# Performance work log

Measured on AMD Instinct MI355X. Metric: run time of the kernel, lower is better.

## Reference

```python
import jax, jax.numpy as jnp
import numpy as np

# module hyperparams (match init_kwargs)
C_IN = 256
HEADS = 8
HEAD_DIM = 32
PW, PH = 4, 4
TOPK = 2
SIM_POW = 2.0
SIDE = 64
T = SIDE * SIDE
B = 16


def setup_inputs() -> dict:
    key = jax.random.key(0)
    ks = jax.random.split(key, 7)
    hd = HEADS * HEAD_DIM
    s = 1.0 / np.sqrt(C_IN)
    return {
        "x": jax.random.normal(ks[0], (T, B, C_IN), dtype=jnp.float32),
        "f_w": jax.random.uniform(ks[1], (hd, C_IN), jnp.float32, -s, s),
        "f_b": jax.random.uniform(ks[2], (hd,), jnp.float32, -s, s),
        "v_w": jax.random.uniform(ks[3], (hd, C_IN), jnp.float32, -s, s),
        "v_b": jax.random.uniform(ks[4], (hd,), jnp.float32, -s, s),
        "proj_w": jax.random.uniform(ks[5], (C_IN, hd), jnp.float32, -1.0 / np.sqrt(hd), 1.0 / np.sqrt(hd)),
        "proj_b": jax.random.uniform(ks[6], (C_IN,), jnp.float32, -1.0 / np.sqrt(hd), 1.0 / np.sqrt(hd)),
        "sim_alpha": jnp.ones((1,), jnp.float32),
        "sim_beta": jnp.zeros((1,), jnp.float32),
    }


def _l2norm(z):
    # F.normalize with eps=1e-12
    n = jnp.linalg.norm(z, axis=-1, keepdims=True)
    return z / jnp.maximum(n, 1e-12)


def reference(x, f_w, f_b, v_w, v_b, proj_w, proj_b, sim_alpha, sim_beta):
    t, b, c = x.shape
    side = SIDE
    H, D = HEADS, HEAD_DIM
    M = PW * PH

    xt = jnp.transpose(x, (1, 0, 2))  # [B, T, C]
    q = xt @ f_w.T + f_b              # [B, T, H*D] (1x1 conv)
    v = xt @ v_w.T + v_b

    def split_heads(z):
        # [B,T,H*D] -> [B*H, side, side, D]
        z = z.reshape(b, side, side, H, D)
        return jnp.transpose(z, (0, 3, 1, 2, 4)).reshape(b * H, side, side, D)

    q2 = split_heads(q)
    v2 = split_heads(v)

    def pool(z):
        # adaptive avg pool (side,side)->(PW,PH), side divisible by PW/PH
        z = z.reshape(b * H, PW, side // PW, PH, side // PH, D)
        return z.mean(axis=(2, 4)).reshape(b * H, M, D)

    centers = pool(q2)        # [BH, M, D]
    value_centers = pool(v2)  # [BH, M, D]
    q_tok = q2.reshape(b * H, t, D)
    v_tok = v2.reshape(b * H, t, D)

    sim = jax.nn.sigmoid(
        sim_beta + sim_alpha * jnp.einsum("bmd,btd->bmt", _l2norm(centers), _l2norm(q_tok))
    )  # [BH, M, T]

    k = min(TOPK, M)
    _, idx = jax.lax.top_k(jnp.transpose(sim, (0, 2, 1)), k)  # idx [BH, T, k] over centers
    mask = jax.nn.one_hot(idx, M, dtype=sim.dtype).sum(axis=2)  # [BH, T, M]
    sim = sim * jnp.transpose(mask, (0, 2, 1))
    if SIM_POW != 1.0:
        sim = sim ** SIM_POW
    sim = sim / (sim.sum(axis=1, keepdims=True) + 1e-6)

    centers_out = (jnp.einsum("bmt,btd->bmd", sim, v_tok) + value_centers) / (
        sim.sum(axis=2, keepdims=True) + 1.0
    )  # [BH, M, D]
    out_tok = jnp.einsum("bmt,bmd->btd", sim, centers_out)  # [BH, T, D]

    out = jnp.transpose(out_tok.reshape(b, H, side, side, D), (0, 2, 3, 1, 4)).reshape(b, t, H * D)
    out = out @ proj_w.T + proj_b  # [B, T, C]
    return jnp.transpose(out, (1, 0, 2))  # [T, B, C]
```

## Files before the change

### kernel.cpp

```cpp
#include <hip/hip_runtime.h>
#include <math.h>

#define T_SZ 4096
#define B_SZ 16
#define CIN 256
#define N_H 8
#define D_H 32
#define M_C 16
#define TAU 5e-5f
#define RCAP (1<<19)

typedef unsigned char u8;
typedef unsigned int uint;
typedef unsigned short ushort;

using frag_ab = __attribute__((ext_vector_type(8))) short;
using frag_c  = __attribute__((ext_vector_type(4))) float;

#define O_FWT   0
#define O_VWT   262144
#define O_WFH   524288
#define O_WFL   655360
#define O_WVH   786432
#define O_WVL   917504
#define O_WPH   1048576
#define O_WPL   1179648
#define O_PX    1310720
#define O_C64   1835008
#define O_C32   2359296
#define O_VC    2621440
#define O_COUT  2883584
#define O_GPART 3145728
#define O_CNT   5308416
#define O_LIST  5308672
#define O_SELM  7405824
#define O_SELW  8454400
#define O_V     12648704

__device__ __forceinline__ uint bfr(float f){
  uint u = __float_as_uint(f);
  return (u + 0x7FFFu + ((u >> 16) & 1u)) >> 16;
}
__device__ __forceinline__ float bff(uint h){ return __uint_as_float(h << 16); }

__global__ void k_transpose(const float* __restrict__ fw, const float* __restrict__ vw,
                            float* __restrict__ fwT, float* __restrict__ vwT){
  int id = blockIdx.x * 256 + threadIdx.x;
  int mat = id >> 16; int rem = id & 65535;
  int j = rem >> 8, c = rem & 255;
  const float* src = (mat == 0) ? fw : vw;
  float* dst = (mat == 0) ? fwT : vwT;
  dst[c * 256 + j] = src[j * 256 + c];
}

__global__ void k_wsplit(const float* __restrict__ fw, const float* __restrict__ vw,
                         const float* __restrict__ pw,
                         ushort* __restrict__ fh, ushort* __restrict__ fl,
                         ushort* __restrict__ vh, ushort* __restrict__ vl,
                         ushort* __restrict__ ph, ushort* __restrict__ pl){
  int id = blockIdx.x * 256 + threadIdx.x;
  int mat = id >> 16, rem = id & 65535;
  const float* s = (mat == 0) ? fw : ((mat == 1) ? vw : pw);
  ushort* dh = (mat == 0) ? fh : ((mat == 1) ? vh : ph);
  ushort* dl = (mat == 0) ? fl : ((mat == 1) ? vl : pl);
  float a = s[rem];
  uint h = bfr(a);
  dh[rem] = (ushort)h;
  dl[rem] = (ushort)bfr(a - bff(h));
}

__global__ void k_pool(const float* __restrict__ x, double* __restrict__ px){
  int b = blockIdx.x >> 4, m = blockIdx.x & 15;
  int pr = m >> 2, pc = m & 3;
  int c = threadIdx.x;
  double s = 0.0;
  for (int i = 0; i < 16; i++){
    int t0 = (pr * 16 + i) * 64 + pc * 16;
    const float* xr = x + ((size_t)t0 * B_SZ + b) * CIN + c;
    for (int jj = 0; jj < 16; jj++)
      s += (double)xr[(size_t)jj * B_SZ * CIN];
  }
  px[(size_t)(b * 16 + m) * 256 + c] = s * (1.0 / 256.0);
}

__global__ void k_centers(const double* __restrict__ px, const float* __restrict__ fwT,
                          const float* __restrict__ vwT, const float* __restrict__ fb,
                          const float* __restrict__ vb, double* __restrict__ c64,
                          float* __restrict__ c32, float* __restrict__ vc){
  int b = blockIdx.x >> 4, m = blockIdx.x & 15;
  int j = threadIdx.x;
  const double* pxr = px + (size_t)(b * 16 + m) * 256;
  double cq = (double)fb[j], cv = (double)vb[j];
  for (int c = 0; c < 256; c++){
    double p = pxr[c];
    cq += p * (double)fwT[c * 256 + j];
    cv += p * (double)vwT[c * 256 + j];
  }
  __shared__ double sq[256];
  __shared__ double snm[8];
  sq[j] = cq * cq;
  __syncthreads();
  int h = j >> 5, d = j & 31;
  if ((j & 31) == 0){
    double ts = 0.0;
    for (int dd = 0; dd < 32; dd++) ts += sq[h * 32 + dd];
    snm[h] = fmax(sqrt(ts), 1e-12);
  }
  __syncthreads();
  double nm = snm[h];
  size_t o = ((size_t)(b * N_H + h) * M_C + m) * D_H + d;
  double ch = cq / nm;
  c64[o] = ch; c32[o] = (float)ch; vc[o] = (float)cv;
}

#define LSTR 40
#define LTILE (128 * LSTR)

__device__ __forceinline__ void stage_tiles(
    const float* __restrict__ A, size_t aBase, int aStride, int kk,
    const ushort* __restrict__ Bh, const ushort* __restrict__ Bl,
    ushort* Ah, ushort* Al, ushort* Bhs, ushort* Bls, int tid){
#pragma unroll
  for (int rep = 0; rep < 2; rep++){
    int part = tid + rep * 256;
    int row = part >> 2, q4 = part & 3;
    const float* ga = A + aBase + (size_t)row * aStride + kk * 32 + q4 * 8;
    float4 a0 = *(const float4*)ga;
    float4 a1 = *(const float4*)(ga + 4);
    uint h0 = bfr(a0.x), h1 = bfr(a0.y), h2 = bfr(a0.z), h3 = bfr(a0.w);
    uint h4 = bfr(a1.x), h5 = bfr(a1.y), h6 = bfr(a1.z), h7 = bfr(a1.w);
    uint l0 = bfr(a0.x - bff(h0)), l1 = bfr(a0.y - bff(h1));
    uint l2 = bfr(a0.z - bff(h2)), l3 = bfr(a0.w - bff(h3));
    uint l4 = bfr(a1.x - bff(h4)), l5 = bfr(a1.y - bff(h5));
    uint l6 = bfr(a1.z - bff(h6)), l7 = bfr(a1.w - bff(h7));
    uint4 hv = make_uint4(h0 | (h1 << 16), h2 | (h3 << 16), h4 | (h5 << 16), h6 | (h7 << 16));
    uint4 lv = make_uint4(l0 | (l1 << 16), l2 | (l3 << 16), l4 | (l5 << 16), l6 | (l7 << 16));
    *(uint4*)&Ah[row * LSTR + q4 * 8] = hv;
    *(uint4*)&Al[row * LSTR + q4 * 8] = lv;
    size_t bo = (size_t)row * 256 + kk * 32 + q4 * 8;
    *(uint4*)&Bhs[row * LSTR + q4 * 8] = *(const uint4*)(Bh + bo);
    *(uint4*)&Bls[row * LSTR + q4 * 8] = *(const uint4*)(Bl + bo);
  }
}

__device__ __forceinline__ void compute_step(
    const ushort* Ah, const ushort* Al, const ushort* Bhs, const ushort* Bls,
    int wm, int wn, int li, int quad, frag_c acc[4][4]){
  frag_ab ah[4], al[4], bh[4], bl[4];
#pragma unroll
  for (int m = 0; m < 4; m++){
    int off = (wm * 64 + m * 16 + li) * LSTR + quad * 8;
    ah[m] = *(const frag_ab*)&Ah[off];
    al[m] = *(const frag_ab*)&Al[off];
  }
#pragma unroll
  for (int n = 0; n < 4; n++){
    int off = (wn * 64 + n * 16 + li) * LSTR + quad * 8;
    bh[n] = *(const frag_ab*)&Bhs[off];
    bl[n] = *(const frag_ab*)&Bls[off];
  }
#pragma unroll
  for (int m = 0; m < 4; m++)
#pragma unroll
    for (int n = 0; n < 4; n++){
      acc[m][n] = __builtin_amdgcn_mfma_f32_16x16x32_bf16(ah[m], bh[n], acc[m][n], 0, 0, 0);
      acc[m][n] = __builtin_amdgcn_mfma_f32_16x16x32_bf16(ah[m], bl[n], acc[m][n], 0, 0, 0);
      acc[m][n] = __builtin_amdgcn_mfma_f32_16x16x32_bf16(al[m], bh[n], acc[m][n], 0, 0, 0);
    }
}

__device__ __forceinline__ void gemm_core(
    const float* __restrict__ A, size_t aBase, int aStride,
    const ushort* __restrict__ Bh, const ushort* __restrict__ Bl,
    ushort* SM, frag_c acc[4][4], int tid){
  ushort* Ah = SM;             ushort* Al = SM + LTILE;
  ushort* Bhs = SM + 2*LTILE;  ushort* Bls = SM + 3*LTILE;
  int li = tid & 15, quad = (tid & 63) >> 4;
  int w = tid >> 6, wm = w >> 1, wn = w & 1;
#pragma unroll
  for (int m = 0; m < 4; m++)
#pragma unroll
    for (int n = 0; n < 4; n++)
      acc[m][n] = frag_c{0.f, 0.f, 0.f, 0.f};
  for (int kk = 0; kk < 8; kk++){
    __syncthreads();
    stage_tiles(A, aBase, aStride, kk, Bh, Bl, Ah, Al, Bhs, Bls, tid);
    __syncthreads();
    compute_step(Ah, Al, Bhs, Bls, wm, wn, li, quad, acc);
  }
}

__global__ __launch_bounds__(256, 3) void k_gemm_store(
    const float* __restrict__ A, int aStride, int aBMul,
    const ushort* __restrict__ Bh, const ushort* __restrict__ Bl,
    const float* __restrict__ bias,
    float* __restrict__ Out, int oStride, int oBMul){
  int bx = blockIdx.x;
  int nt = bx & 1, mt = (bx >> 1) & 31, b = bx >> 6;
  __shared__ ushort SM[4 * LTILE];
  frag_c acc[4][4];
  int tid = threadIdx.x;
  size_t aBase = (size_t)b * aBMul + (size_t)(mt * 128) * aStride;
  const ushort* Bhp = Bh + (size_t)(nt * 128) * 256;
  const ushort* Blp = Bl + (size_t)(nt * 128) * 256;
  gemm_core(A, aBase, aStride, Bhp, Blp, SM, acc, tid);

  int li = tid & 15, quad = (tid & 63) >> 4;
  int w = tid >> 6, wm = w >> 1, wn = w & 1;
  int colBase = nt * 128 + wn * 64 + li;
  float bn[4];
#pragma unroll
  for (int n = 0; n < 4; n++) bn[n] = bias[colBase + n * 16];
#pragma unroll
  for (int m = 0; m < 4; m++){
    int row0 = mt * 128 + wm * 64 + m * 16 + quad * 4;
#pragma unroll
    for (int n = 0; n < 4; n++){
      int col = colBase + n * 16;
#pragma unroll
      for (int r = 0; r < 4; r++)
        Out[(size_t)(row0 + r) * oStride + (size_t)b * oBMul + col] = acc[m][n][r] + bn[n];
    }
  }
}

__global__ __launch_bounds__(256, 2) void k_gemm_qsim(
    const float* __restrict__ A, int aStride, int aBMul,
    const ushort* __restrict__ Bh, const ushort* __restrict__ Bl,
    const float* __restrict__ bias, const float* __restrict__ c32,
    const float* __restrict__ salpha, const float* __restrict__ sbeta,
    u8* __restrict__ selm, float2* __restrict__ selw,
    int* __restrict__ cnt, unsigned int* __restrict__ list){
  int bx = blockIdx.x;
  int nt = bx & 1, mt = (bx >> 1) & 31, b = bx >> 6;
  __shared__ ushort SM[4 * LTILE];
  __shared__ float cs[4][520];
  frag_c acc[4][4];
  int tid = threadIdx.x;
  for (int i = tid; i < 2048; i += 256){
    int hh = i >> 9, rem = i & 511;
    cs[hh][rem] = c32[(size_t)b * 4096 + (nt * 4 + hh) * 512 + rem];
  }
  size_t aBase = (size_t)b * aBMul + (size_t)(mt * 128) * aStride;
  const ushort* Bhp = Bh + (size_t)(nt * 128) * 256;
  const ushort* Blp = Bl + (size_t)(nt * 128) * 256;
  gemm_core(A, aBase, aStride, Bhp, Blp, SM, acc, tid);

  int li = tid & 15, quad = (tid & 63) >> 4;
  int w = tid >> 6, wm = w >> 1, wn = w & 1;
  int colBase = nt * 128 + wn * 64 + li;
  float bn[4];
#pragma unroll
  for (int n = 0; n < 4; n++) bn[n] = bias[colBase + n * 16];
  float alpha = salpha[0], beta = sbeta[0];
  float* qbuf = (float*)SM;
  for (int half = 0; half < 2; half++){
    __syncthreads();
    if (wm == half){
#pragma unroll
      for (int m = 0; m < 4; m++)
#pragma unroll
        for (int n = 0; n < 4; n++)
#pragma unroll
          for (int r = 0; r < 4; r++)
            qbuf[(m * 16 + quad * 4 + r) * 132 + wn * 64 + n * 16 + li] = acc[m][n][r] + bn[n];
    }
    __syncthreads();
    int tok = tid >> 2, hh = tid & 3;
    int t = mt * 128 + half * 64 + tok;
    int h = nt * 4 + hh;
    float q[32];
    float ss = 0.f;
#pragma unroll
    for (int d = 0; d < 32; d += 4){
      float4 qv = *(const float4*)&qbuf[tok * 132 + hh * 32 + d];
      q[d] = qv.x; q[d + 1] = qv.y; q[d + 2] = qv.z; q[d + 3] = qv.w;
      ss += qv.x * qv.x + qv.y * qv.y + qv.z * qv.z + qv.w * qv.w;
    }
    float inv = 1.f / fmaxf(sqrtf(ss), 1e-12f);
    float s1 = -1e30f, s2 = -1e30f, s3 = -1e30f; int i1 = 0, i2 = 0;
#pragma unroll
    for (int m = 0; m < 16; m++){
      float dot = 0.f;
#pragma unroll
      for (int d = 0; d < 32; d += 4){
        float4 cv = *(const float4*)&cs[hh][m * 32 + d];
        dot = fmaf(q[d], cv.x, fmaf(q[d + 1], cv.y, fmaf(q[d + 2], cv.z, fmaf(q[d + 3], cv.w, dot))));
      }
      float z = beta + alpha * (dot * inv);
      float s = 1.f / (1.f + expf(-z));
      if (s > s1){ s3 = s2; s2 = s1; i2 = i1; s1 = s; i1 = m; }
      else if (s > s2){ s3 = s2; s2 = s; i2 = m; }
      else if (s > s3){ s3 = s; }
    }
    if (s2 - s3 < TAU){
      int idx = atomicAdd(cnt, 1);
      if (idx < RCAP) list[idx] = (((unsigned)(b * N_H + h)) << 12) | (unsigned)t;
    }
    float r1 = s1 * s1, r2 = s2 * s2;
    float den = r1 + r2 + 1e-6f;
    size_t so = (size_t)(b * N_H + h) * T_SZ + t;
    selm[so * 2] = (u8)i1; selm[so * 2 + 1] = (u8)i2;
    selw[so] = make_float2(r1 / den, r2 / den);
  }
}

__global__ __launch_bounds__(256, 4) void k_rescue(
    const float* __restrict__ x, const float* __restrict__ fw, const float* __restrict__ fb,
    const double* __restrict__ c64, const float* __restrict__ salpha, const float* __restrict__ sbeta,
    const int* __restrict__ cnt, const unsigned int* __restrict__ list,
    u8* __restrict__ selm, float2* __restrict__ selw){
  int n = *cnt; if (n > RCAP) n = RCAP;
  int lane = threadIdx.x & 63;
  int wid = (blockIdx.x * 256 + threadIdx.x) >> 6;
  int nw = gridDim.x * 4;
  double alpha = (double)salpha[0], beta = (double)sbeta[0];
  for (int i = wid; i < n; i += nw){
    unsigned e = list[i];
    int t = e & 4095; int bh = e >> 12; int b = bh >> 3, h = bh & 7;
    int d = lane & 31, half = lane >> 5;
    const float* xh = x + ((size_t)t * B_SZ + b) * CIN + half * 128;
    const float* wr = fw + (size_t)(h * 32 + d) * CIN + half * 128;
    double a0 = 0, a1 = 0, a2 = 0, a3 = 0;
#pragma unroll 4
    for (int c = 0; c < 128; c += 4){
      float4 xv = *(const float4*)(xh + c);
      float4 wv = *(const float4*)(wr + c);
      a0 += (double)xv.x * (double)wv.x;
      a1 += (double)xv.y * (double)wv.y;
      a2 += (double)xv.z * (double)wv.z;
      a3 += (double)xv.w * (double)wv.w;
    }
    double qd = (a0 + a1) + (a2 + a3);
    qd += __shfl_down(qd, 32);
    if (lane < 32) qd += (double)fb[h * 32 + d];
    else qd = 0.0;
    double ss = qd * qd;
#pragma unroll
    for (int off = 32; off; off >>= 1) ss += __shfl_xor(ss, off);
    double inv = 1.0 / fmax(sqrt(ss), 1e-12);
    const double* cb = c64 + (size_t)bh * (M_C * D_H);
    int m = lane & 15;
    double dot = 0.0;
#pragma unroll
    for (int dd = 0; dd < 32; dd++){
      double qv = __shfl(qd, dd);
      dot += qv * cb[m * 32 + dd];
    }
    double z = beta + alpha * (dot * inv);
    double s = 1.0 / (1.0 + exp(-z));
    double s1 = -1e300, s2 = -1e300; int i1 = 0, i2 = 0;
#pragma unroll
    for (int mm = 0; mm < 16; mm++){
      double sv = __shfl(s, mm);
      if (sv > s1){ s2 = s1; i2 = i1; s1 = sv; i1 = mm; }
      else if (sv > s2){ s2 = sv; i2 = mm; }
    }
    if (lane == 0){
      double r1 = s1 * s1, r2 = s2 * s2, den = r1 + r2 + 1e-6;
      size_t so = (size_t)bh * T_SZ + t;
      selm[so * 2] = (u8)i1; selm[so * 2 + 1] = (u8)i2;
      selw[so] = make_float2((float)(r1 / den), (float)(r2 / den));
    }
  }
}

__global__ __launch_bounds__(256, 4) void k_scatter(
    const float* __restrict__ v, const u8* __restrict__ selm, const float2* __restrict__ selw,
    float* __restrict__ gpart){
  int bh = blockIdx.x >> 3, chunk = blockIdx.x & 7;
  int b = bh >> 3, h = bh & 7;
  int tid = threadIdx.x;
  int mA = tid >> 5, mB = mA + 8, d = tid & 31;
  __shared__ uchar2 sm[512];
  __shared__ float2 sw[512];
  for (int i = tid; i < 512; i += 256){
    size_t so = (size_t)bh * T_SZ + chunk * 512 + i;
    sm[i] = make_uchar2(selm[so * 2], selm[so * 2 + 1]);
    sw[i] = selw[so];
  }
  __syncthreads();
  const float* vb = v + ((size_t)b * T_SZ + chunk * 512) * CIN + h * 32 + d;
  float accA = 0.f, accB = 0.f, cntA = 0.f, cntB = 0.f;
#pragma unroll 8
  for (int i = 0; i < 512; i++){
    float vv = vb[(size_t)i * CIN];
    uchar2 mm = sm[i];
    float2 w = sw[i];
    float wA = (mm.x == mA) ? w.x : ((mm.y == mA) ? w.y : 0.f);
    float wB = (mm.x == mB) ? w.x : ((mm.y == mB) ? w.y : 0.f);
    accA = fmaf(wA, vv, accA); cntA += wA;
    accB = fmaf(wB, vv, accB); cntB += wB;
  }
  float* gp = gpart + (size_t)(bh * 8 + chunk) * 528;
  gp[mA * 33 + d] = accA;
  gp[mB * 33 + d] = accB;
  if (d == 0){ gp[mA * 33 + 32] = cntA; gp[mB * 33 + 32] = cntB; }
}

__global__ void k_cfinal(const float* __restrict__ gpart, const float* __restrict__ vc,
                         float* __restrict__ cout){
  int id = blockIdx.x * 256 + threadIdx.x;
  int bh = id >> 9, rem = id & 511, m = rem >> 5, d = rem & 31;
  float num = 0.f, den = 0.f;
#pragma unroll
  for (int c = 0; c < 8; c++){
    const float* gp = gpart + (size_t)(bh * 8 + c) * 528 + m * 33;
    num += gp[d];
    den += gp[32];
  }
  cout[id] = (num + vc[id]) / (den + 1.0f);
}

__global__ __launch_bounds__(256, 4) void k_mix(
    const float* __restrict__ cout, const u8* __restrict__ selm, const float2* __restrict__ selw,
    float* __restrict__ OT){
  int b = blockIdx.x >> 7, tt = blockIdx.x & 127;
  __shared__ float cs[8][516];
  int tid = threadIdx.x;
  for (int k = 0; k < 16; k++){
    int i = k * 256 + tid;
    cs[i >> 9][i & 511] = cout[(size_t)b * 4096 + i];
  }
  __syncthreads();
  int r = tid >> 3, h = tid & 7;
  int t = tt * 32 + r;
  size_t so = (size_t)(b * N_H + h) * T_SZ + t;
  int m1 = selm[so * 2], m2 = selm[so * 2 + 1];
  float2 w = selw[so];
#pragma unroll
  for (int d = 0; d < 32; d += 4){
    float4 c1 = *(const float4*)&cs[h][m1 * 32 + d];
    float4 c2 = *(const float4*)&cs[h][m2 * 32 + d];
    float4 o = make_float4(w.x * c1.x + w.y * c2.x, w.x * c1.y + w.y * c2.y,
                           w.x * c1.z + w.y * c2.z, w.x * c1.w + w.y * c2.w);
    *(float4*)&OT[((size_t)b * T_SZ + t) * CIN + h * 32 + d] = o;
  }
}

extern "C" void kernel_launch(void* const* d_in, const int* in_sizes, int n_in,
                              void* d_out, int out_size, void* d_ws, size_t ws_size,
                              hipStream_t stream) {
  const float* x   = (const float*)d_in[0];
  const float* f_w = (const float*)d_in[1];
  const float* f_b = (const float*)d_in[2];
  const float* v_w = (const float*)d_in[3];
  const float* v_b = (const float*)d_in[4];
  const float* p_w = (const float*)d_in[5];
  const float* p_b = (const float*)d_in[6];
  const float* s_a = (const float*)d_in[7];
  const float* s_b = (const float*)d_in[8];
  float* out = (float*)d_out;
  char* ws = (char*)d_ws;

  float*  fwT  = (float*)(ws + O_FWT);
  float*  vwT  = (float*)(ws + O_VWT);
  ushort* wfh  = (ushort*)(ws + O_WFH);
  ushort* wfl  = (ushort*)(ws + O_WFL);
  ushort* wvh  = (ushort*)(ws + O_WVH);
  ushort* wvl  = (ushort*)(ws + O_WVL);
  ushort* wph  = (ushort*)(ws + O_WPH);
  ushort* wpl  = (ushort*)(ws + O_WPL);
  double* px   = (double*)(ws + O_PX);
  double* c64  = (double*)(ws + O_C64);
  float*  c32  = (float*)(ws + O_C32);
  float*  vc   = (float*)(ws + O_VC);
  float*  cout = (float*)(ws + O_COUT);
  float*  gpart= (float*)(ws + O_GPART);
  int*    cnt  = (int*)(ws + O_CNT);
  unsigned int* list = (unsigned int*)(ws + O_LIST);
  u8*     selm = (u8*)(ws + O_SELM);
  float2* selw = (float2*)(ws + O_SELW);
  float*  v    = (float*)(ws + O_V);
  float*  OT   = (float*)(ws + O_V);

  hipMemsetAsync(ws + O_CNT, 0, 256, stream);
  k_transpose<<<512, 256, 0, stream>>>(f_w, v_w, fwT, vwT);
  k_wsplit<<<768, 256, 0, stream>>>(f_w, v_w, p_w, wfh, wfl, wvh, wvl, wph, wpl);
  k_pool<<<256, 256, 0, stream>>>(x, px);
  k_centers<<<256, 256, 0, stream>>>(px, fwT, vwT, f_b, v_b, c64, c32, vc);
  k_gemm_qsim<<<1024, 256, 0, stream>>>(x, 4096, 256, wfh, wfl, f_b, c32, s_a, s_b,
                                        selm, selw, cnt, list);
  k_gemm_store<<<1024, 256, 0, stream>>>(x, 4096, 256, wvh, wvl, v_b, v, 256, T_SZ * CIN);
  k_rescue<<<256, 256, 0, stream>>>(x, f_w, f_b, c64, s_a, s_b, cnt, list, selm, selw);
  k_scatter<<<1024, 256, 0, stream>>>(v, selm, selw, gpart);
  k_cfinal<<<256, 256, 0, stream>>>(gpart, vc, cout);
  k_mix<<<2048, 256, 0, stream>>>(cout, selm, selw, OT);
  k_gemm_store<<<1024, 256, 0, stream>>>(OT, 256, T_SZ * CIN, wph, wpl, p_b, out, 4096, 256);
}
```

Measured before the change: 399.4 us.

## Pre-split activations to bf16 hi/lo and stage GEMM tiles via direct global-to-LDS loads

A new pass converts x into bf16 high/low planes in batch-major layout once, and k_mix writes its output directly as bf16 hi/lo, so the GEMM kernels no longer convert fp32 tiles during staging. Tile staging now uses global_load_lds so each wave copies one of the four operand tiles straight into LDS in a k-chunk-major layout, without a register round trip. The cost is an extra full pass over x that writes two 32 MB buffers, plus a larger workspace. Synchronisation is still a plain load-then-barrier with no double buffering.

```diff
diff --git a/kernel.cpp b/kernel.cpp
--- a/kernel.cpp
+++ b/kernel.cpp
@@ -35,7 +35,9 @@
 #define O_LIST  5308672
 #define O_SELM  7405824
 #define O_SELW  8454400
-#define O_V     12648704
+#define O_XS    12648704
+#define O_XSL   46203136
+#define O_V     79757568
 
 __device__ __forceinline__ uint bfr(float f){
   uint u = __float_as_uint(f);
@@ -69,6 +71,20 @@
   dl[rem] = (ushort)bfr(a - bff(h));
 }
 
+__global__ __launch_bounds__(256, 8) void k_xsplit(
+    const float* __restrict__ x, ushort* __restrict__ xh, ushort* __restrict__ xl){
+  size_t gid = (size_t)blockIdx.x * 256 + threadIdx.x;
+  size_t o = gid * 4;
+  int c = (int)(o & 255); size_t bt = o >> 8;
+  int t = (int)(bt & 4095); int b = (int)(bt >> 12);
+  float4 a = *(const float4*)(x + ((size_t)t * B_SZ + b) * CIN + c);
+  uint h0 = bfr(a.x), h1 = bfr(a.y), h2 = bfr(a.z), h3 = bfr(a.w);
+  uint l0 = bfr(a.x - bff(h0)), l1 = bfr(a.y - bff(h1));
+  uint l2 = bfr(a.z - bff(h2)), l3 = bfr(a.w - bff(h3));
+  *(uint2*)(xh + o) = make_uint2(h0 | (h1 << 16), h2 | (h3 << 16));
+  *(uint2*)(xl + o) = make_uint2(l0 | (l1 << 16), l2 | (l3 << 16));
+}
+
 __global__ void k_pool(const float* __restrict__ x, double* __restrict__ px){
   int b = blockIdx.x >> 4, m = blockIdx.x & 15;
   int pr = m >> 2, pc = m & 3;
@@ -113,51 +129,42 @@
   c64[o] = ch; c32[o] = (float)ch; vc[o] = (float)cv;
 }
 
-#define LSTR 40
-#define LTILE (128 * LSTR)
-
-__device__ __forceinline__ void stage_tiles(
-    const float* __restrict__ A, size_t aBase, int aStride, int kk,
-    const ushort* __restrict__ Bh, const ushort* __restrict__ Bl,
-    ushort* Ah, ushort* Al, ushort* Bhs, ushort* Bls, int tid){
-#pragma unroll
-  for (int rep = 0; rep < 2; rep++){
-    int part = tid + rep * 256;
-    int row = part >> 2, q4 = part & 3;
-    const float* ga = A + aBase + (size_t)row * aStride + kk * 32 + q4 * 8;
-    float4 a0 = *(const float4*)ga;
-    float4 a1 = *(const float4*)(ga + 4);
-    uint h0 = bfr(a0.x), h1 = bfr(a0.y), h2 = bfr(a0.z), h3 = bfr(a0.w);
-    uint h4 = bfr(a1.x), h5 = bfr(a1.y), h6 = bfr(a1.z), h7 = bfr(a1.w);
-    uint l0 = bfr(a0.x - bff(h0)), l1 = bfr(a0.y - bff(h1));
-    uint l2 = bfr(a0.z - bff(h2)), l3 = bfr(a0.w - bff(h3));
-    uint l4 = bfr(a1.x - bff(h4)), l5 = bfr(a1.y - bff(h5));
-    uint l6 = bfr(a1.z - bff(h6)), l7 = bfr(a1.w - bff(h7));
-    uint4 hv = make_uint4(h0 | (h1 << 16), h2 | (h3 << 16), h4 | (h5 << 16), h6 | (h7 << 16));
-    uint4 lv = make_uint4(l0 | (l1 << 16), l2 | (l3 << 16), l4 | (l5 << 16), l6 | (l7 << 16));
-    *(uint4*)&Ah[row * LSTR + q4 * 8] = hv;
-    *(uint4*)&Al[row * LSTR + q4 * 8] = lv;
-    size_t bo = (size_t)row * 256 + kk * 32 + q4 * 8;
-    *(uint4*)&Bhs[row * LSTR + q4 * 8] = *(const uint4*)(Bh + bo);
-    *(uint4*)&Bls[row * LSTR + q4 * 8] = *(const uint4*)(Bl + bo);
+#define TSZU 4096
+
+__device__ __forceinline__ void stage_async(
+    const ushort* __restrict__ Ahg, const ushort* __restrict__ Alg, size_t aRow0,
+    const ushort* __restrict__ Bhg, const ushort* __restrict__ Blg, int bRow0,
+    int kk, ushort* SM, int tid){
+  int w = tid >> 6, lane = tid & 63;
+  const ushort* src = (w == 0) ? Ahg : (w == 1) ? Alg : (w == 2) ? Bhg : Blg;
+  size_t row0 = (w < 2) ? aRow0 : (size_t)bRow0;
+  ushort* dst = SM + w * TSZU;
+#pragma unroll
+  for (int j = 0; j < 8; j++){
+    int kchunk = j >> 1, rh = j & 1;
+    const ushort* g = src + (row0 + (size_t)(rh * 64 + lane)) * 256 + kk * 32 + kchunk * 8;
+    ushort* l = dst + (kchunk * 128 + rh * 64) * 8;
+    __builtin_amdgcn_global_load_lds((const __attribute__((address_space(1))) void*)g,
+                                     (__attribute__((address_space(3))) void*)l, 16, 0, 0);
   }
 }
 
 __device__ __forceinline__ void compute_step(
-    const ushort* Ah, const ushort* Al, const ushort* Bhs, const ushort* Bls,
-    int wm, int wn, int li, int quad, frag_c acc[4][4]){
+    const ushort* SM, int wm, int wn, int li, int quad, frag_c acc[4][4]){
+  const ushort* Ah = SM;            const ushort* Al = SM + TSZU;
+  const ushort* Bh = SM + 2*TSZU;   const ushort* Bl = SM + 3*TSZU;
   frag_ab ah[4], al[4], bh[4], bl[4];
 #pragma unroll
   for (int m = 0; m < 4; m++){
-    int off = (wm * 64 + m * 16 + li) * LSTR + quad * 8;
+    int off = (quad * 128 + wm * 64 + m * 16 + li) * 8;
     ah[m] = *(const frag_ab*)&Ah[off];
     al[m] = *(const frag_ab*)&Al[off];
   }
 #pragma unroll
   for (int n = 0; n < 4; n++){
-    int off = (wn * 64 + n * 16 + li) * LSTR + quad * 8;
-    bh[n] = *(const frag_ab*)&Bhs[off];
-    bl[n] = *(const frag_ab*)&Bls[off];
+    int off = (quad * 128 + wn * 64 + n * 16 + li) * 8;
+    bh[n] = *(const frag_ab*)&Bh[off];
+    bl[n] = *(const frag_ab*)&Bl[off];
   }
 #pragma unroll
   for (int m = 0; m < 4; m++)
@@ -170,11 +177,9 @@
 }
 
 __device__ __forceinline__ void gemm_core(
-    const float* __restrict__ A, size_t aBase, int aStride,
-    const ushort* __restrict__ Bh, const ushort* __restrict__ Bl,
+    const ushort* __restrict__ Ahg, const ushort* __restrict__ Alg, size_t aRow0,
+    const ushort* __restrict__ Bhg, const ushort* __restrict__ Blg, int bRow0,
     ushort* SM, frag_c acc[4][4], int tid){
-  ushort* Ah = SM;             ushort* Al = SM + LTILE;
-  ushort* Bhs = SM + 2*LTILE;  ushort* Bls = SM + 3*LTILE;
   int li = tid & 15, quad = (tid & 63) >> 4;
   int w = tid >> 6, wm = w >> 1, wn = w & 1;
 #pragma unroll
@@ -184,26 +189,23 @@
       acc[m][n] = frag_c{0.f, 0.f, 0.f, 0.f};
   for (int kk = 0; kk < 8; kk++){
     __syncthreads();
-    stage_tiles(A, aBase, aStride, kk, Bh, Bl, Ah, Al, Bhs, Bls, tid);
+    stage_async(Ahg, Alg, aRow0, Bhg, Blg, bRow0, kk, SM, tid);
     __syncthreads();
-    compute_step(Ah, Al, Bhs, Bls, wm, wn, li, quad, acc);
+    compute_step(SM, wm, wn, li, quad, acc);
   }
 }
 
 __global__ __launch_bounds__(256, 3) void k_gemm_store(
-    const float* __restrict__ A, int aStride, int aBMul,
+    const ushort* __restrict__ Ahg, const ushort* __restrict__ Alg,
     const ushort* __restrict__ Bh, const ushort* __restrict__ Bl,
     const float* __restrict__ bias,
     float* __restrict__ Out, int oStride, int oBMul){
   int bx = blockIdx.x;
   int nt = bx & 1, mt = (bx >> 1) & 31, b = bx >> 6;
-  __shared__ ushort SM[4 * LTILE];
+  __shared__ ushort SM[4 * TSZU];
   frag_c acc[4][4];
   int tid = threadIdx.x;
-  size_t aBase = (size_t)b * aBMul + (size_t)(mt * 128) * aStride;
-  const ushort* Bhp = Bh + (size_t)(nt * 128) * 256;
-  const ushort* Blp = Bl + (size_t)(nt * 128) * 256;
-  gemm_core(A, aBase, aStride, Bhp, Blp, SM, acc, tid);
+  gemm_core(Ahg, Alg, (size_t)b * 4096 + mt * 128, Bh, Bl, nt * 128, SM, acc, tid);
 
   int li = tid & 15, quad = (tid & 63) >> 4;
   int w = tid >> 6, wm = w >> 1, wn = w & 1;
@@ -225,7 +227,7 @@
 }
 
 __global__ __launch_bounds__(256, 2) void k_gemm_qsim(
-    const float* __restrict__ A, int aStride, int aBMul,
+    const ushort* __restrict__ Ahg, const ushort* __restrict__ Alg,
     const ushort* __restrict__ Bh, const ushort* __restrict__ Bl,
     const float* __restrict__ bias, const float* __restrict__ c32,
     const float* __restrict__ salpha, const float* __restrict__ sbeta,
@@ -233,7 +235,7 @@
     int* __restrict__ cnt, unsigned int* __restrict__ list){
   int bx = blockIdx.x;
   int nt = bx & 1, mt = (bx >> 1) & 31, b = bx >> 6;
-  __shared__ ushort SM[4 * LTILE];
+  __shared__ ushort SM[16896];
   __shared__ float cs[4][520];
   frag_c acc[4][4];
   int tid = threadIdx.x;
@@ -241,10 +243,7 @@
     int hh = i >> 9, rem = i & 511;
     cs[hh][rem] = c32[(size_t)b * 4096 + (nt * 4 + hh) * 512 + rem];
   }
-  size_t aBase = (size_t)b * aBMul + (size_t)(mt * 128) * aStride;
-  const ushort* Bhp = Bh + (size_t)(nt * 128) * 256;
-  const ushort* Blp = Bl + (size_t)(nt * 128) * 256;
-  gemm_core(A, aBase, aStride, Bhp, Blp, SM, acc, tid);
+  gemm_core(Ahg, Alg, (size_t)b * 4096 + mt * 128, Bh, Bl, nt * 128, SM, acc, tid);
 
   int li = tid & 15, quad = (tid & 63) >> 4;
   int w = tid >> 6, wm = w >> 1, wn = w & 1;
@@ -414,7 +413,7 @@
 
 __global__ __launch_bounds__(256, 4) void k_mix(
     const float* __restrict__ cout, const u8* __restrict__ selm, const float2* __restrict__ selw,
-    float* __restrict__ OT){
+    ushort* __restrict__ OTh, ushort* __restrict__ OTl){
   int b = blockIdx.x >> 7, tt = blockIdx.x & 127;
   __shared__ float cs[8][516];
   int tid = threadIdx.x;
@@ -434,7 +433,12 @@
     float4 c2 = *(const float4*)&cs[h][m2 * 32 + d];
     float4 o = make_float4(w.x * c1.x + w.y * c2.x, w.x * c1.y + w.y * c2.y,
                            w.x * c1.z + w.y * c2.z, w.x * c1.w + w.y * c2.w);
-    *(float4*)&OT[((size_t)b * T_SZ + t) * CIN + h * 32 + d] = o;
+    uint h0 = bfr(o.x), h1 = bfr(o.y), h2 = bfr(o.z), h3 = bfr(o.w);
+    uint l0 = bfr(o.x - bff(h0)), l1 = bfr(o.y - bff(h1));
+    uint l2 = bfr(o.z - bff(h2)), l3 = bfr(o.w - bff(h3));
+    size_t oo = ((size_t)b * T_SZ + t) * CIN + h * 32 + d;
+    *(uint2*)(OTh + oo) = make_uint2(h0 | (h1 << 16), h2 | (h3 << 16));
+    *(uint2*)(OTl + oo) = make_uint2(l0 | (l1 << 16), l2 | (l3 << 16));
   }
 }
 
@@ -471,20 +475,24 @@
   unsigned int* list = (unsigned int*)(ws + O_LIST);
   u8*     selm = (u8*)(ws + O_SELM);
   float2* selw = (float2*)(ws + O_SELW);
+  ushort* xh   = (ushort*)(ws + O_XS);
+  ushort* xl   = (ushort*)(ws + O_XSL);
+  ushort* OTh  = (ushort*)(ws + O_XS);
+  ushort* OTl  = (ushort*)(ws + O_XSL);
   float*  v    = (float*)(ws + O_V);
-  float*  OT   = (float*)(ws + O_V);
 
   hipMemsetAsync(ws + O_CNT, 0, 256, stream);
   k_transpose<<<512, 256, 0, stream>>>(f_w, v_w, fwT, vwT);
   k_wsplit<<<768, 256, 0, stream>>>(f_w, v_w, p_w, wfh, wfl, wvh, wvl, wph, wpl);
+  k_xsplit<<<16384, 256, 0, stream>>>(x, xh, xl);
   k_pool<<<256, 256, 0, stream>>>(x, px);
   k_centers<<<256, 256, 0, stream>>>(px, fwT, vwT, f_b, v_b, c64, c32, vc);
-  k_gemm_qsim<<<1024, 256, 0, stream>>>(x, 4096, 256, wfh, wfl, f_b, c32, s_a, s_b,
+  k_gemm_qsim<<<1024, 256, 0, stream>>>(xh, xl, wfh, wfl, f_b, c32, s_a, s_b,
                                         selm, selw, cnt, list);
-  k_gemm_store<<<1024, 256, 0, stream>>>(x, 4096, 256, wvh, wvl, v_b, v, 256, T_SZ * CIN);
+  k_gemm_store<<<1024, 256, 0, stream>>>(xh, xl, wvh, wvl, v_b, v, 256, T_SZ * CIN);
   k_rescue<<<256, 256, 0, stream>>>(x, f_w, f_b, c64, s_a, s_b, cnt, list, selm, selw);
   k_scatter<<<1024, 256, 0, stream>>>(v, selm, selw, gpart);
   k_cfinal<<<256, 256, 0, stream>>>(gpart, vc, cout);
-  k_mix<<<2048, 256, 0, stream>>>(cout, selm, selw, OT);
-  k_gemm_store<<<1024, 256, 0, stream>>>(OT, 256, T_SZ * CIN, wph, wpl, p_b, out, 4096, 256);
-}
+  k_mix<<<2048, 256, 0, stream>>>(cout, selm, selw, OTh, OTl);
+  k_gemm_store<<<1024, 256, 0, stream>>>(OTh, OTl, wph, wpl, p_b, out, 4096, 256);
+}
```

New measurement: 498.5 us. 1.25x slower.
